# Kernel tuning notes

Measured on AMD Instinct MI355X. Metric: run time of the kernel, lower is better.

## Reference

```python
import jax, jax.numpy as jnp
import numpy as np

T, B, IN, H = 1024, 128, 256, 512


def setup_inputs() -> dict:
    key = jax.random.key(0)
    k1, k2, k3, k4, k5 = jax.random.split(key, 5)
    s = 1.0 / np.sqrt(H)  # PyTorch LSTM init scale
    return {
        "x": jax.random.normal(k1, (T, B, IN), dtype=jnp.float32),
        "W_ih": jax.random.normal(k2, (4 * H, IN), dtype=jnp.float32) * s,
        "W_hh": jax.random.normal(k3, (4 * H, H), dtype=jnp.float32) * s,
        "b_ih": jax.random.normal(k4, (4 * H,), dtype=jnp.float32) * s,
        "b_hh": jax.random.normal(k5, (4 * H,), dtype=jnp.float32) * s,
    }


def reference(x, W_ih, W_hh, b_ih, b_hh):
    # Single-layer unidirectional LSTM scanned over the full sequence.
    # PyTorch gate order within the 4H dim: i, f, g, o.
    b = b_ih + b_hh
    Wx = jnp.einsum('tbi,gi->tbg', x, W_ih) + b  # precompute input projection [T,B,4H]

    def step(carry, zx):
        h, c = carry
        z = zx + h @ W_hh.T  # [B, 4H]
        i, f, g, o = jnp.split(z, 4, axis=-1)
        i = jax.nn.sigmoid(i)
        f = jax.nn.sigmoid(f)
        g = jnp.tanh(g)
        o = jax.nn.sigmoid(o)
        c = f * c + i * g
        h = o * jnp.tanh(c)
        return (h, c), None

    h0 = jnp.zeros((B, H), dtype=x.dtype)
    c0 = jnp.zeros((B, H), dtype=x.dtype)
    (h, c), _ = jax.lax.scan(step, (h0, c0), Wx)
    # Original returns the LAST step's output plus (h_n, c_n); with 1 layer output == h_n.
    output = h[None]          # [1, B, H]
    h_n = h[None]             # [num_layers=1, B, H]
    c_n = c[None]
    return (output, h_n, c_n)
```

## Files before the change

### kernel.cpp

```cpp
#include <hip/hip_runtime.h>
#include <hip/hip_bf16.h>

typedef __attribute__((ext_vector_type(8)))  short short8;
typedef __attribute__((ext_vector_type(16))) float f32x16;
typedef __attribute__((ext_vector_type(4)))  unsigned int uint4v;

#define TSTEPS 1024
#define BATCH  128
#define NIN    256
#define NHID   512
#define GM     4
#define MBLK   32
#define XPSTR  528
#define XBUF   8448
#define HSTR   520
#define HBUF   16640

__device__ __forceinline__ unsigned short f2bf(float f) {
  unsigned int u = __builtin_bit_cast(unsigned int, f);
  u += 0x7fffu + ((u >> 16) & 1u);
  return (unsigned short)(u >> 16);
}

__device__ __forceinline__ unsigned long long pack4(float a, float b, float c, float d) {
  return (unsigned long long)f2bf(a)
       | ((unsigned long long)f2bf(b) << 16)
       | ((unsigned long long)f2bf(c) << 32)
       | ((unsigned long long)f2bf(d) << 48);
}

__device__ __forceinline__ float sigf(float x) {
  return 1.0f / (1.0f + __expf(-x));
}
__device__ __forceinline__ float tanh_fast(float x) {
  x = fminf(fmaxf(x, -15.0f), 15.0f);
  float e = __expf(2.0f * x);
  return (e - 1.0f) / (e + 1.0f);
}

__global__ void init_ws_kernel(unsigned long long* tbuf) {
  int idx = blockIdx.x * blockDim.x + threadIdx.x;
  for (int i = idx; i < 65536; i += 16384) tbuf[i] = 0ull;
}

__global__ void convert_x_kernel(const float* __restrict__ x, unsigned short* __restrict__ xbf) {
  const int N4 = TSTEPS * BATCH * NIN / 4;
  for (int i = blockIdx.x * blockDim.x + threadIdx.x; i < N4; i += gridDim.x * blockDim.x) {
    float4 f = *(const float4*)(x + (size_t)i * 4);
    *(unsigned long long*)(xbf + (size_t)i * 4) = pack4(f.x, f.y, f.z, f.w);
  }
}

#define MFMA(va, fb, acc) \
  acc = __builtin_amdgcn_mfma_f32_32x32x16_bf16(va, fb, acc, 0, 0, 0)

#define CLOAD(cv, off) \
  asm volatile("global_load_dwordx4 %0, %1, off sc1" : "=v"(cv) : "v"(rb + (off)))

template <int USE_DMA>
__global__ __launch_bounds__(256, 1) void lstm_persistent(
    const float* __restrict__ x,
    const unsigned short* __restrict__ xbf,
    const float* __restrict__ Wih,
    const float* __restrict__ Whh,
    const float* __restrict__ bih,
    const float* __restrict__ bhh,
    float* __restrict__ out,
    char* __restrict__ tbuf)
{
  const int tid  = threadIdx.x;
  const int lane = tid & 63;
  const int wv   = tid >> 6;
  const int gm   = blockIdx.x & (GM - 1);
  const int gh   = blockIdx.x >> 2;
  const int m0   = gm * MBLK;
  const int hc0  = gh * 32;

  __shared__ short x_flat[3 * XBUF];
  __shared__ short h_flat[2 * HBUF];
  __shared__ float z_lds[4][MBLK][36];

  const int ncol = lane & 31;
  const int h5   = lane >> 5;
  const int arow = lane & 31;
  const int kg   = h5 * 8;
  const int gate = ncol >> 3;
  const int wrow = gate * NHID + hc0 + wv * 8 + (ncol & 7);

  short8 bfrag[48];
#pragma unroll
  for (int kb = 0; kb < 48; ++kb) {
    const float* src = (kb < 16)
        ? (Wih + (size_t)wrow * NIN  + (kb * 16 + kg))
        : (Whh + (size_t)wrow * NHID + (kb * 16 + kg - NIN));
    float4 f0 = *(const float4*)src;
    float4 f1 = *(const float4*)(src + 4);
    short8 b;
    b[0] = (short)f2bf(f0.x); b[1] = (short)f2bf(f0.y);
    b[2] = (short)f2bf(f0.z); b[3] = (short)f2bf(f0.w);
    b[4] = (short)f2bf(f1.x); b[5] = (short)f2bf(f1.y);
    b[6] = (short)f2bf(f1.z); b[7] = (short)f2bf(f1.w);
    bfrag[kb] = b;
  }
  const float bias_c = bih[wrow] + bhh[wrow];

  const int grow = tid >> 3;
  const int c4   = (tid & 7) * 4;
  float creg[4] = {0.0f, 0.0f, 0.0f, 0.0f};

  const char* tb = tbuf + (size_t)gm * 131072;
  const int  myci = grow * 128 + (hc0 >> 2) + (tid & 7);

#define XLOAD(i, v) { int u = tid + 256 * (i); \
    v = *(const float4*)(xt + (size_t)(u >> 6) * NIN + (u & 63) * 4); }
#define XPACK(bb, i, v) { int u = tid + 256 * (i); int r = u >> 6; int hc = u & 63; \
    *(unsigned long long*)&x_flat[(bb) * XBUF + (r >> 1) * XPSTR + (r & 1) * NIN + hc * 4] \
        = pack4(v.x, v.y, v.z, v.w); }
#define XDMA(tt, bb) { \
    const unsigned short* gsrc = xbf + ((size_t)(tt) * BATCH + m0) * NIN; \
    short* ldst = x_flat + (bb) * XBUF; \
    _Pragma("unroll") \
    for (int j = 0; j < 4; ++j) { \
      int ck = 4 * wv + j; \
      const unsigned short* gp = gsrc + (size_t)(2 * ck + h5) * NIN + (lane & 31) * 8; \
      __builtin_amdgcn_global_load_lds((const unsigned int*)gp, \
          (unsigned int*)(ldst + ck * XPSTR), 16, 0, 0); \
    } }

  f32x16 a0, a1, a2, a3;
  float4 xv0, xv1, xv2, xv3, xv4, xv5, xv6, xv7;

  if (USE_DMA) {
    XDMA(0, 0) XDMA(1, 1) XDMA(2, 2)
    asm volatile("s_waitcnt vmcnt(0)" ::: "memory");
  } else {
    { const float* xt = x + (size_t)m0 * NIN;
      XLOAD(0, xv0) XLOAD(1, xv1) XLOAD(2, xv2) XLOAD(3, xv3)
      XLOAD(4, xv4) XLOAD(5, xv5) XLOAD(6, xv6) XLOAD(7, xv7)
      XPACK(0, 0, xv0) XPACK(0, 1, xv1) XPACK(0, 2, xv2) XPACK(0, 3, xv3)
      XPACK(0, 4, xv4) XPACK(0, 5, xv5) XPACK(0, 6, xv6) XPACK(0, 7, xv7) }
    { const float* xt = x + ((size_t)BATCH + m0) * NIN;
      XLOAD(0, xv0) XLOAD(1, xv1) XLOAD(2, xv2) XLOAD(3, xv3)
      XLOAD(4, xv4) XLOAD(5, xv5) XLOAD(6, xv6) XLOAD(7, xv7)
      XPACK(1, 0, xv0) XPACK(1, 1, xv1) XPACK(1, 2, xv2) XPACK(1, 3, xv3)
      XPACK(1, 4, xv4) XPACK(1, 5, xv5) XPACK(1, 6, xv6) XPACK(1, 7, xv7) }
  }
  __syncthreads();
  a0 = (f32x16)bias_c; a1 = (f32x16)0.0f; a2 = (f32x16)0.0f; a3 = (f32x16)0.0f;
  {
    const short* xrow = x_flat + (arow >> 1) * XPSTR + (arow & 1) * NIN + kg;
#pragma unroll
    for (int kb = 0; kb < 16; kb += 4) {
      MFMA(*(const short8*)(xrow + (kb + 0) * 16), bfrag[kb + 0], a0);
      MFMA(*(const short8*)(xrow + (kb + 1) * 16), bfrag[kb + 1], a1);
      MFMA(*(const short8*)(xrow + (kb + 2) * 16), bfrag[kb + 2], a2);
      MFMA(*(const short8*)(xrow + (kb + 3) * 16), bfrag[kb + 3], a3);
    }
  }

  int tmod = 0;
  for (int t = 0; t < TSTEPS; ++t) {
    {
      const char* rb = tb + (size_t)(t & 1) * 65536 + (size_t)tid * 16;
      const unsigned int tg = (unsigned int)t;
      uint4v c0, c1, c2, c3, c4v, c5, c6, c7, c8, c9, c10, c11, c12, c13, c14, c15;
      int ok;
      do {
        CLOAD(c0,  0 * 4096); CLOAD(c1,  1 * 4096); CLOAD(c2,  2 * 4096);
        CLOAD(c3,  3 * 4096); CLOAD(c4v, 4 * 4096); CLOAD(c5,  5 * 4096);
        CLOAD(c6,  6 * 4096); CLOAD(c7,  7 * 4096); CLOAD(c8,  8 * 4096);
        CLOAD(c9,  9 * 4096); CLOAD(c10, 10 * 4096); CLOAD(c11, 11 * 4096);
        CLOAD(c12, 12 * 4096); CLOAD(c13, 13 * 4096); CLOAD(c14, 14 * 4096);
        CLOAD(c15, 15 * 4096);
        asm volatile("s_waitcnt vmcnt(0)" ::: "memory");
        ok = (c0.z == tg) & (c1.z == tg) & (c2.z == tg) & (c3.z == tg)
           & (c4v.z == tg) & (c5.z == tg) & (c6.z == tg) & (c7.z == tg)
           & (c8.z == tg) & (c9.z == tg) & (c10.z == tg) & (c11.z == tg)
           & (c12.z == tg) & (c13.z == tg) & (c14.z == tg) & (c15.z == tg);
      } while (!__all(ok));
      __builtin_amdgcn_sched_barrier(0);
      short* hdst = h_flat + (t & 1) * HBUF;
#define HPUT(j, cv) { int ci = tid + 256 * (j); \
      *(unsigned long long*)&hdst[(ci >> 7) * HSTR + (ci & 127) * 4] = \
          (unsigned long long)cv.x | ((unsigned long long)cv.y << 32); }
      HPUT(0, c0)  HPUT(1, c1)  HPUT(2, c2)  HPUT(3, c3)
      HPUT(4, c4v) HPUT(5, c5)  HPUT(6, c6)  HPUT(7, c7)
      HPUT(8, c8)  HPUT(9, c9)  HPUT(10, c10) HPUT(11, c11)
      HPUT(12, c12) HPUT(13, c13) HPUT(14, c14) HPUT(15, c15)
#undef HPUT
    }
    __syncthreads();

    if (!USE_DMA && t + 2 < TSTEPS) {
      const float* xt = x + ((size_t)(t + 2) * BATCH + m0) * NIN;
      XLOAD(0, xv0) XLOAD(1, xv1) XLOAD(2, xv2) XLOAD(3, xv3)
      XLOAD(4, xv4) XLOAD(5, xv5) XLOAD(6, xv6) XLOAD(7, xv7)
    }

    {
      const short* hrow = h_flat + (t & 1) * HBUF + arow * HSTR + kg;
#pragma unroll
      for (int kb = 0; kb < 32; kb += 4) {
        MFMA(*(const short8*)(hrow + (kb + 0) * 16), bfrag[16 + kb + 0], a0);
        MFMA(*(const short8*)(hrow + (kb + 1) * 16), bfrag[16 + kb + 1], a1);
        MFMA(*(const short8*)(hrow + (kb + 2) * 16), bfrag[16 + kb + 2], a2);
        MFMA(*(const short8*)(hrow + (kb + 3) * 16), bfrag[16 + kb + 3], a3);
      }
    }

    {
      f32x16 acc = (a0 + a1) + (a2 + a3);
#pragma unroll
      for (int r = 0; r < 16; ++r) {
        int zr = (r & 3) + 8 * (r >> 2) + 4 * h5;
        z_lds[wv][zr][ncol] = acc[r];
      }
    }
    __syncthreads();

    {
      const int wz = c4 >> 3;
      const int cc = c4 & 7;
      const float* zrow = &z_lds[wz][grow][0];
      float4 vi = *(const float4*)&zrow[ 0 + cc];
      float4 vf = *(const float4*)&zrow[ 8 + cc];
      float4 vg = *(const float4*)&zrow[16 + cc];
      float4 vo = *(const float4*)&zrow[24 + cc];
      float zi[4] = {vi.x, vi.y, vi.z, vi.w};
      float zf[4] = {vf.x, vf.y, vf.z, vf.w};
      float zg[4] = {vg.x, vg.y, vg.z, vg.w};
      float zo[4] = {vo.x, vo.y, vo.z, vo.w};
      float hnv[4];
#pragma unroll
      for (int u = 0; u < 4; ++u) {
        float iv = sigf(zi[u]);
        float fv = sigf(zf[u]);
        float gv = tanh_fast(zg[u]);
        float ov = sigf(zo[u]);
        float cn = fv * creg[u] + iv * gv;
        creg[u] = cn;
        hnv[u] = ov * tanh_fast(cn);
      }
      if (t == TSTEPS - 1) {
        size_t o = (size_t)(m0 + grow) * NHID + hc0 + c4;
        float4 hq; hq.x = hnv[0]; hq.y = hnv[1]; hq.z = hnv[2]; hq.w = hnv[3];
        float4 cq; cq.x = creg[0]; cq.y = creg[1]; cq.z = creg[2]; cq.w = creg[3];
        *(float4*)&out[o]          = hq;
        *(float4*)&out[65536 + o]  = hq;
        *(float4*)&out[131072 + o] = cq;
      } else {
        unsigned long long hp = pack4(hnv[0], hnv[1], hnv[2], hnv[3]);
        uint4v sv;
        sv.x = (unsigned int)hp;
        sv.y = (unsigned int)(hp >> 32);
        sv.z = (unsigned int)(t + 1);
        sv.w = 0u;
        const char* wb = tb + (size_t)((t + 1) & 1) * 65536 + (size_t)myci * 16;
        asm volatile("global_store_dwordx4 %0, %1, off sc1"
                     :: "v"(wb), "v"(sv) : "memory");
      }
    }

    if (t < TSTEPS - 1) {
      if (USE_DMA) {
        if (t + 3 < TSTEPS) { XDMA(t + 3, tmod) }
      } else if (t + 2 < TSTEPS) {
        int pb = tmod + 2; if (pb >= 3) pb -= 3;
        XPACK(pb, 0, xv0) XPACK(pb, 1, xv1) XPACK(pb, 2, xv2) XPACK(pb, 3, xv3)
        XPACK(pb, 4, xv4) XPACK(pb, 5, xv5) XPACK(pb, 6, xv6) XPACK(pb, 7, xv7)
      }
      int nb = tmod + 1; if (nb >= 3) nb -= 3;
      a0 = (f32x16)bias_c; a1 = (f32x16)0.0f; a2 = (f32x16)0.0f; a3 = (f32x16)0.0f;
      const short* xrow = x_flat + nb * XBUF + (arow >> 1) * XPSTR + (arow & 1) * NIN + kg;
#pragma unroll
      for (int kb = 0; kb < 16; kb += 4) {
        MFMA(*(const short8*)(xrow + (kb + 0) * 16), bfrag[kb + 0], a0);
        MFMA(*(const short8*)(xrow + (kb + 1) * 16), bfrag[kb + 1], a1);
        MFMA(*(const short8*)(xrow + (kb + 2) * 16), bfrag[kb + 2], a2);
        MFMA(*(const short8*)(xrow + (kb + 3) * 16), bfrag[kb + 3], a3);
      }
    }
    tmod = tmod + 1; if (tmod >= 3) tmod = 0;
  }
#undef XLOAD
#undef XPACK
#undef XDMA
}

extern "C" void kernel_launch(void* const* d_in, const int* in_sizes, int n_in,
                              void* d_out, int out_size, void* d_ws, size_t ws_size,
                              hipStream_t stream) {
  const float* x   = (const float*)d_in[0];
  const float* Wih = (const float*)d_in[1];
  const float* Whh = (const float*)d_in[2];
  const float* bih = (const float*)d_in[3];
  const float* bhh = (const float*)d_in[4];
  float* out = (float*)d_out;

  char* tbuf = (char*)d_ws;
  unsigned short* xbf = (unsigned short*)((char*)d_ws + (1 << 20));

  size_t need = (size_t)(1 << 20) + (size_t)TSTEPS * BATCH * NIN * 2;
  bool dma = ws_size >= need;

  hipLaunchKernelGGL(init_ws_kernel, dim3(64), dim3(256), 0, stream,
                     (unsigned long long*)tbuf);
  if (dma) {
    hipLaunchKernelGGL(convert_x_kernel, dim3(8192), dim3(256), 0, stream, x, xbf);
    hipLaunchKernelGGL((lstm_persistent<1>), dim3(64), dim3(256), 0, stream,
                       x, xbf, Wih, Whh, bih, bhh, out, tbuf);
  } else {
    hipLaunchKernelGGL((lstm_persistent<0>), dim3(64), dim3(256), 0, stream,
                       x, xbf, Wih, Whh, bih, bhh, out, tbuf);
  }
}
```

Baseline: 3.385 ms.

## Split h exchange into separate data and per-wave flag, load MFMA fragments directly from global

Inter-block hidden-state exchange now uses a compact per-wave tag array that each wave polls with one dword load, instead of polling 16 tagged 16-byte records per thread. The h data is stored in MFMA fragment layout in global memory, so each wave streams its A operands straight into registers in pipelined batches overlapping the recurrent MFMAs. This removes the LDS h staging and one block barrier per step, and z_lds is double-buffered to stay safe without that barrier. In exchange, writers need a store-wait-then-flag protocol, and correctness relies on ordering across the two stores.

```diff
diff --git a/kernel.cpp b/kernel.cpp
--- a/kernel.cpp
+++ b/kernel.cpp
@@ -13,8 +13,13 @@
 #define MBLK   32
 #define XPSTR  528
 #define XBUF   8448
-#define HSTR   520
-#define HBUF   16640
+
+#define DSLOT  32768
+#define DGRP   65536
+#define TAGOFF 262144
+#define TGRP   8192
+#define TSLOT  4096
+#define ZBYTES 294912
 
 __device__ __forceinline__ unsigned short f2bf(float f) {
   unsigned int u = __builtin_bit_cast(unsigned int, f);
@@ -38,9 +43,9 @@
   return (e - 1.0f) / (e + 1.0f);
 }
 
-__global__ void init_ws_kernel(unsigned long long* tbuf) {
+__global__ void init_ws_kernel(unsigned long long* w) {
   int idx = blockIdx.x * blockDim.x + threadIdx.x;
-  for (int i = idx; i < 65536; i += 16384) tbuf[i] = 0ull;
+  for (int i = idx; i < ZBYTES / 8; i += 16384) w[i] = 0ull;
 }
 
 __global__ void convert_x_kernel(const float* __restrict__ x, unsigned short* __restrict__ xbf) {
@@ -53,9 +58,19 @@
 
 #define MFMA(va, fb, acc) \
   acc = __builtin_amdgcn_mfma_f32_32x32x16_bf16(va, fb, acc, 0, 0, 0)
-
-#define CLOAD(cv, off) \
-  asm volatile("global_load_dwordx4 %0, %1, off sc1" : "=v"(cv) : "v"(rb + (off)))
+#define MF(r, b, acc) \
+  acc = __builtin_amdgcn_mfma_f32_32x32x16_bf16(__builtin_bit_cast(short8, r), b, acc, 0, 0, 0)
+
+#define HISSUE(r, kb_) \
+  asm volatile("global_load_dwordx4 %0, %1, off sc1" : "=v"(r) : "v"(hb + (kb_) * 1024))
+#define VMW(n) do { asm volatile("s_waitcnt vmcnt(" #n ")" ::: "memory"); \
+  __builtin_amdgcn_sched_barrier(0); } while (0)
+
+#define CONS8(r0,r1,r2,r3,r4,r5,r6,r7, B) \
+  MF(r0, bfrag[(B)+0], a0); MF(r1, bfrag[(B)+1], a1); \
+  MF(r2, bfrag[(B)+2], a2); MF(r3, bfrag[(B)+3], a3); \
+  MF(r4, bfrag[(B)+4], a0); MF(r5, bfrag[(B)+5], a1); \
+  MF(r6, bfrag[(B)+6], a2); MF(r7, bfrag[(B)+7], a3);
 
 template <int USE_DMA>
 __global__ __launch_bounds__(256, 1) void lstm_persistent(
@@ -66,7 +81,7 @@
     const float* __restrict__ bih,
     const float* __restrict__ bhh,
     float* __restrict__ out,
-    char* __restrict__ tbuf)
+    char* __restrict__ ws)
 {
   const int tid  = threadIdx.x;
   const int lane = tid & 63;
@@ -77,8 +92,7 @@
   const int hc0  = gh * 32;
 
   __shared__ short x_flat[3 * XBUF];
-  __shared__ short h_flat[2 * HBUF];
-  __shared__ float z_lds[4][MBLK][36];
+  __shared__ float z_lds[2][4][MBLK][36];
 
   const int ncol = lane & 31;
   const int h5   = lane >> 5;
@@ -108,8 +122,11 @@
   const int c4   = (tid & 7) * 4;
   float creg[4] = {0.0f, 0.0f, 0.0f, 0.0f};
 
-  const char* tb = tbuf + (size_t)gm * 131072;
-  const int  myci = grow * 128 + (hc0 >> 2) + (tid & 7);
+  char* db = ws + gm * DGRP;
+  char* tb = ws + TAGOFF + gm * TGRP;
+  const int frago = (lane & 31) * 32 + h5 * 16;
+  const int mytag = gh * 4 + wv;
+  const int pso = (2 * gh + (c4 >> 4)) * 1024 + grow * 32 + ((c4 >> 3) & 1) * 16 + (c4 & 7) * 2;
 
 #define XLOAD(i, v) { int u = tid + 256 * (i); \
     v = *(const float4*)(xt + (size_t)(u >> 6) * NIN + (u & 63) * 4); }
@@ -161,35 +178,37 @@
   int tmod = 0;
   for (int t = 0; t < TSTEPS; ++t) {
     {
-      const char* rb = tb + (size_t)(t & 1) * 65536 + (size_t)tid * 16;
-      const unsigned int tg = (unsigned int)t;
-      uint4v c0, c1, c2, c3, c4v, c5, c6, c7, c8, c9, c10, c11, c12, c13, c14, c15;
-      int ok;
+      const char* tp = tb + (t & 1) * TSLOT + lane * 64;
+      unsigned int tv;
       do {
-        CLOAD(c0,  0 * 4096); CLOAD(c1,  1 * 4096); CLOAD(c2,  2 * 4096);
-        CLOAD(c3,  3 * 4096); CLOAD(c4v, 4 * 4096); CLOAD(c5,  5 * 4096);
-        CLOAD(c6,  6 * 4096); CLOAD(c7,  7 * 4096); CLOAD(c8,  8 * 4096);
-        CLOAD(c9,  9 * 4096); CLOAD(c10, 10 * 4096); CLOAD(c11, 11 * 4096);
-        CLOAD(c12, 12 * 4096); CLOAD(c13, 13 * 4096); CLOAD(c14, 14 * 4096);
-        CLOAD(c15, 15 * 4096);
+        asm volatile("global_load_dword %0, %1, off sc1" : "=v"(tv) : "v"(tp));
         asm volatile("s_waitcnt vmcnt(0)" ::: "memory");
-        ok = (c0.z == tg) & (c1.z == tg) & (c2.z == tg) & (c3.z == tg)
-           & (c4v.z == tg) & (c5.z == tg) & (c6.z == tg) & (c7.z == tg)
-           & (c8.z == tg) & (c9.z == tg) & (c10.z == tg) & (c11.z == tg)
-           & (c12.z == tg) & (c13.z == tg) & (c14.z == tg) & (c15.z == tg);
-      } while (!__all(ok));
+      } while (!__all((int)(tv >= (unsigned int)t)));
       __builtin_amdgcn_sched_barrier(0);
-      short* hdst = h_flat + (t & 1) * HBUF;
-#define HPUT(j, cv) { int ci = tid + 256 * (j); \
-      *(unsigned long long*)&hdst[(ci >> 7) * HSTR + (ci & 127) * 4] = \
-          (unsigned long long)cv.x | ((unsigned long long)cv.y << 32); }
-      HPUT(0, c0)  HPUT(1, c1)  HPUT(2, c2)  HPUT(3, c3)
-      HPUT(4, c4v) HPUT(5, c5)  HPUT(6, c6)  HPUT(7, c7)
-      HPUT(8, c8)  HPUT(9, c9)  HPUT(10, c10) HPUT(11, c11)
-      HPUT(12, c12) HPUT(13, c13) HPUT(14, c14) HPUT(15, c15)
-#undef HPUT
-    }
-    __syncthreads();
+    }
+
+    {
+      const char* hb = db + (t & 1) * DSLOT + frago;
+      uint4v h0, h1, h2, h3, h4, h5v, h6, h7;
+      uint4v h8, h9, h10, h11, h12, h13, h14, h15;
+      uint4v h16, h17, h18, h19, h20, h21, h22, h23;
+      HISSUE(h0, 0);   HISSUE(h1, 1);   HISSUE(h2, 2);   HISSUE(h3, 3);
+      HISSUE(h4, 4);   HISSUE(h5v, 5);  HISSUE(h6, 6);   HISSUE(h7, 7);
+      HISSUE(h8, 8);   HISSUE(h9, 9);   HISSUE(h10, 10); HISSUE(h11, 11);
+      HISSUE(h12, 12); HISSUE(h13, 13); HISSUE(h14, 14); HISSUE(h15, 15);
+      HISSUE(h16, 16); HISSUE(h17, 17); HISSUE(h18, 18); HISSUE(h19, 19);
+      HISSUE(h20, 20); HISSUE(h21, 21); HISSUE(h22, 22); HISSUE(h23, 23);
+      VMW(16);
+      CONS8(h0, h1, h2, h3, h4, h5v, h6, h7, 16)
+      HISSUE(h0, 24);  HISSUE(h1, 25);  HISSUE(h2, 26);  HISSUE(h3, 27);
+      HISSUE(h4, 28);  HISSUE(h5v, 29); HISSUE(h6, 30);  HISSUE(h7, 31);
+      VMW(16);
+      CONS8(h8, h9, h10, h11, h12, h13, h14, h15, 24)
+      VMW(8);
+      CONS8(h16, h17, h18, h19, h20, h21, h22, h23, 32)
+      VMW(0);
+      CONS8(h0, h1, h2, h3, h4, h5v, h6, h7, 40)
+    }
 
     if (!USE_DMA && t + 2 < TSTEPS) {
       const float* xt = x + ((size_t)(t + 2) * BATCH + m0) * NIN;
@@ -198,22 +217,11 @@
     }
 
     {
-      const short* hrow = h_flat + (t & 1) * HBUF + arow * HSTR + kg;
-#pragma unroll
-      for (int kb = 0; kb < 32; kb += 4) {
-        MFMA(*(const short8*)(hrow + (kb + 0) * 16), bfrag[16 + kb + 0], a0);
-        MFMA(*(const short8*)(hrow + (kb + 1) * 16), bfrag[16 + kb + 1], a1);
-        MFMA(*(const short8*)(hrow + (kb + 2) * 16), bfrag[16 + kb + 2], a2);
-        MFMA(*(const short8*)(hrow + (kb + 3) * 16), bfrag[16 + kb + 3], a3);
-      }
-    }
-
-    {
       f32x16 acc = (a0 + a1) + (a2 + a3);
 #pragma unroll
       for (int r = 0; r < 16; ++r) {
         int zr = (r & 3) + 8 * (r >> 2) + 4 * h5;
-        z_lds[wv][zr][ncol] = acc[r];
+        z_lds[t & 1][wv][zr][ncol] = acc[r];
       }
     }
     __syncthreads();
@@ -221,7 +229,7 @@
     {
       const int wz = c4 >> 3;
       const int cc = c4 & 7;
-      const float* zrow = &z_lds[wz][grow][0];
+      const float* zrow = &z_lds[t & 1][wz][grow][0];
       float4 vi = *(const float4*)&zrow[ 0 + cc];
       float4 vf = *(const float4*)&zrow[ 8 + cc];
       float4 vg = *(const float4*)&zrow[16 + cc];
@@ -250,14 +258,16 @@
         *(float4*)&out[131072 + o] = cq;
       } else {
         unsigned long long hp = pack4(hnv[0], hnv[1], hnv[2], hnv[3]);
-        uint4v sv;
-        sv.x = (unsigned int)hp;
-        sv.y = (unsigned int)(hp >> 32);
-        sv.z = (unsigned int)(t + 1);
-        sv.w = 0u;
-        const char* wb = tb + (size_t)((t + 1) & 1) * 65536 + (size_t)myci * 16;
-        asm volatile("global_store_dwordx4 %0, %1, off sc1"
-                     :: "v"(wb), "v"(sv) : "memory");
+        char* pd = db + ((t + 1) & 1) * DSLOT + pso;
+        asm volatile("global_store_dwordx2 %0, %1, off sc1"
+                     :: "v"(pd), "v"(hp) : "memory");
+        asm volatile("s_waitcnt vmcnt(0)" ::: "memory");
+        if (lane == 0) {
+          unsigned int tg = (unsigned int)(t + 1);
+          char* tp = tb + ((t + 1) & 1) * TSLOT + mytag * 64;
+          asm volatile("global_store_dword %0, %1, off sc1"
+                       :: "v"(tp), "v"(tg) : "memory");
+        }
       }
     }
 
@@ -297,20 +307,20 @@
   const float* bhh = (const float*)d_in[4];
   float* out = (float*)d_out;
 
-  char* tbuf = (char*)d_ws;
-  unsigned short* xbf = (unsigned short*)((char*)d_ws + (1 << 20));
+  char* ws = (char*)d_ws;
+  unsigned short* xbf = (unsigned short*)(ws + (1 << 20));
 
   size_t need = (size_t)(1 << 20) + (size_t)TSTEPS * BATCH * NIN * 2;
   bool dma = ws_size >= need;
 
   hipLaunchKernelGGL(init_ws_kernel, dim3(64), dim3(256), 0, stream,
-                     (unsigned long long*)tbuf);
+                     (unsigned long long*)ws);
   if (dma) {
     hipLaunchKernelGGL(convert_x_kernel, dim3(8192), dim3(256), 0, stream, x, xbf);
     hipLaunchKernelGGL((lstm_persistent<1>), dim3(64), dim3(256), 0, stream,
-                       x, xbf, Wih, Whh, bih, bhh, out, tbuf);
+                       x, xbf, Wih, Whh, bih, bhh, out, ws);
   } else {
     hipLaunchKernelGGL((lstm_persistent<0>), dim3(64), dim3(256), 0, stream,
-                       x, xbf, Wih, Whh, bih, bhh, out, tbuf);
-  }
-}
+                       x, xbf, Wih, Whh, bih, bhh, out, ws);
+  }
+}
```

Result: slower. 3.683 ms (+8.8%).
